# Kernel optimization log

Hardware: AMD Instinct MI355X
Metric: run time of the kernel (lower is better)

The kernel has to match this reference:

```python
import jax, jax.numpy as jnp
import numpy as np

N, C, H, W = 4, 32, 384, 1280
DISP_SCALE = 20.0  # realistic disparity magnitudes


def setup_inputs() -> dict:
    key = jax.random.key(0)
    k1, k2 = jax.random.split(key)
    img = jax.random.normal(k1, (N, C, H, W), dtype=jnp.float32)
    disp = jax.random.normal(k2, (N, 1, H, W), dtype=jnp.float32) * DISP_SCALE
    return {"img": img, "disp": disp}


def _warp_bilinear_zeros(img, disp):
    # Faithful translation of Warp1DOp.warp_by_disparity_map with
    # mode='bilinear', padding_mode='zeros', align_corners=True.
    n, c, h, w = img.shape
    # x-coordinate grid minus disparity: (n, 1, h, w)
    x = jnp.arange(w, dtype=img.dtype)[None, None, None, :] - disp
    # zeros padding: clip to [-1, w] then shift by +1 (indices into padded img)
    x = jnp.clip(x, -1.0, jnp.asarray(w, img.dtype)) + 1.0
    # pad coord map and image by one zero column on each side of W
    x = jnp.pad(x, ((0, 0), (0, 0), (0, 0), (1, 1)))          # (n,1,h,w+2)
    imgp = jnp.pad(img, ((0, 0), (0, 0), (0, 0), (1, 1)))      # (n,c,h,w+2)
    x0 = jnp.floor(x).astype(jnp.int32)
    x1 = jnp.ceil(x).astype(jnp.int32)
    dx = x - x0.astype(img.dtype)
    idx_shape = (n, c, h, w + 2)
    v_x0 = jnp.take_along_axis(imgp, jnp.broadcast_to(x0, idx_shape), axis=-1)
    v_x1 = jnp.take_along_axis(imgp, jnp.broadcast_to(x1, idx_shape), axis=-1)
    warped = (1.0 - dx) * v_x0 + dx * v_x1
    # strip padding columns
    return warped[:, :, :, 1:-1]


def reference(img, disp):
    return _warp_bilinear_zeros(img, disp)
```

## Files before the change

kernel.cpp:

```cpp
#include <hip/hip_runtime.h>

#define N_ 4
#define C_ 32
#define H_ 384
#define W_ 1280
#define WP_ (W_ + 8)

__device__ __forceinline__ void stage16(const float* g, float* l) {
    __builtin_amdgcn_global_load_lds(
        (const __attribute__((address_space(1))) void*)g,
        (__attribute__((address_space(3))) void*)l, 16, 0, 0);
}

__global__ __launch_bounds__(320) void warp1d_kernel(
    const float* __restrict__ img,
    const float* __restrict__ disp,
    float* __restrict__ out)
{
    __shared__ float buf[2][WP_];

    const int tid  = threadIdx.x;
    const int nh   = blockIdx.x;
    const int w0   = tid * 4;
    const int lane = tid & 63;
    const int wave = tid >> 6;
    const int chunk = wave * 256 + lane * 4;

    if (tid < 16) {
        const int b = tid >> 3;
        const int z = tid & 7;
        buf[b][(z < 4) ? z : (W_ + z)] = 0.0f;
    }

    const float4 d4 = *(const float4*)(disp + (long)nh * W_ + w0);
    const float dv[4] = {d4.x, d4.y, d4.z, d4.w};

    int   ix[4];
    float fx[4], wa[4];
#pragma unroll
    for (int j = 0; j < 4; ++j) {
        float x = (float)(w0 + j) - dv[j];
        x = fminf(fmaxf(x, -1.0f), (float)W_) + 1.0f;
        const float xf = floorf(x);
        fx[j] = x - xf;
        wa[j] = 1.0f - fx[j];
        ix[j] = (int)xf + 3;
    }

    const int  n = nh / H_;
    const int  h = nh % H_;
    const long rowbase = ((long)n * C_ * H_ + h) * W_;
    const float* gsrc = img + rowbase + chunk;
    float*       gdst = out + rowbase + w0;

    stage16(gsrc, &buf[0][4 + wave * 256]);
    gsrc += (long)H_ * W_;
    __syncthreads();

#pragma unroll 2
    for (int c = 0; c < C_; ++c) {
        if (c + 1 < C_) {
            stage16(gsrc, &buf[(c + 1) & 1][4 + wave * 256]);
            gsrc += (long)H_ * W_;
        }
        const float* __restrict__ r = buf[c & 1];
        float4 o;
        float* op = (float*)&o;
#pragma unroll
        for (int j = 0; j < 4; ++j) {
            const float v0 = r[ix[j]];
            const float v1 = r[ix[j] + 1];
            op[j] = fmaf(fx[j], v1, wa[j] * v0);
        }
        *(float4*)gdst = o;
        gdst += (long)H_ * W_;
        __syncthreads();
    }
}

extern "C" void kernel_launch(void* const* d_in, const int* in_sizes, int n_in,
                              void* d_out, int out_size, void* d_ws, size_t ws_size,
                              hipStream_t stream) {
    const float* img  = (const float*)d_in[0];
    const float* disp = (const float*)d_in[1];
    float* out = (float*)d_out;

    constexpr int grid  = N_ * H_;
    constexpr int block = 320;

    warp1d_kernel<<<grid, block, 0, stream>>>(img, disp, out);
}
```

Before: 427.0 us.

## Triple-buffer LDS staging with two-channel prefetch and explicit vmcnt waits

Moves from double to triple buffering of the per-channel image row in LDS, so two channels are prefetched ahead of the one being computed. Each iteration now has a single barrier, placed after an explicit `s_waitcnt vmcnt`, instead of a trailing `__syncthreads`. The channel loop is fully unrolled with compile-time buffer indices. The aim is to hide more global-load latency in this latency-bound streaming kernel, at the cost of more LDS per block and hand-tuned wait counts that depend on how loads and stores are ordered in vmcnt.

```diff
diff --git a/kernel.cpp b/kernel.cpp
--- a/kernel.cpp
+++ b/kernel.cpp
@@ -17,7 +17,7 @@
     const float* __restrict__ disp,
     float* __restrict__ out)
 {
-    __shared__ float buf[2][WP_];
+    __shared__ float buf[3][WP_];
 
     const int tid  = threadIdx.x;
     const int nh   = blockIdx.x;
@@ -26,7 +26,7 @@
     const int wave = tid >> 6;
     const int chunk = wave * 256 + lane * 4;
 
-    if (tid < 16) {
+    if (tid < 24) {
         const int b = tid >> 3;
         const int z = tid & 7;
         buf[b][(z < 4) ? z : (W_ + z)] = 0.0f;
@@ -49,33 +49,39 @@
 
     const int  n = nh / H_;
     const int  h = nh % H_;
+    const long HW = (long)H_ * W_;
     const long rowbase = ((long)n * C_ * H_ + h) * W_;
-    const float* gsrc = img + rowbase + chunk;
-    float*       gdst = out + rowbase + w0;
 
-    stage16(gsrc, &buf[0][4 + wave * 256]);
-    gsrc += (long)H_ * W_;
-    __syncthreads();
+#define STAGE_CH(c) \
+    stage16(img + rowbase + (long)(c) * HW + chunk, &buf[(c) % 3][4 + wave * 256])
 
-#pragma unroll 2
-    for (int c = 0; c < C_; ++c) {
-        if (c + 1 < C_) {
-            stage16(gsrc, &buf[(c + 1) & 1][4 + wave * 256]);
-            gsrc += (long)H_ * W_;
-        }
-        const float* __restrict__ r = buf[c & 1];
-        float4 o;
-        float* op = (float*)&o;
+    STAGE_CH(0);
+    STAGE_CH(1);
+    asm volatile("s_waitcnt lgkmcnt(0)" ::: "memory");
+
+#define BODY(c, VM) do {                                                      \
+    asm volatile("s_waitcnt vmcnt(" #VM ")" ::: "memory");                    \
+    __builtin_amdgcn_s_barrier();                                             \
+    asm volatile("" ::: "memory");      \
+    if ((c) + 2 < C_) { STAGE_CH((c) + 2); }                                  \
+    asm volatile("" ::: "memory");    \
+    const float* __restrict__ r = buf[(c) % 3];                               \
+    float4 o; float* op = (float*)&o;                                         \
+    op[0] = fmaf(fx[0], r[ix[0] + 1], wa[0] * r[ix[0]]);                      \
+    op[1] = fmaf(fx[1], r[ix[1] + 1], wa[1] * r[ix[1]]);                      \
+    op[2] = fmaf(fx[2], r[ix[2] + 1], wa[2] * r[ix[2]]);                      \
+    op[3] = fmaf(fx[3], r[ix[3] + 1], wa[3] * r[ix[3]]);                      \
+    *(float4*)(out + rowbase + (long)(c) * HW + w0) = o;                      \
+} while (0)
+
+    BODY(0, 1);
+    BODY(1, 2);
 #pragma unroll
-        for (int j = 0; j < 4; ++j) {
-            const float v0 = r[ix[j]];
-            const float v1 = r[ix[j] + 1];
-            op[j] = fmaf(fx[j], v1, wa[j] * v0);
-        }
-        *(float4*)gdst = o;
-        gdst += (long)H_ * W_;
-        __syncthreads();
-    }
+    for (int c = 2; c <= 30; ++c) BODY(c, 2);
+    BODY(31, 1);
+
+#undef BODY
+#undef STAGE_CH
 }
 
 extern "C" void kernel_launch(void* const* d_in, const int* in_sizes, int n_in,
```

Measured after the change: 415.2 us. 1.03x faster.
